# Optimization experiments

Measured on AMD Instinct MI355X. Metric: run time of the kernel, lower is better.

Reference implementation:

```python
import jax, jax.numpy as jnp
import numpy as np

D_MODEL = 512
N_HEADS = 8
HEAD_DIM = D_MODEL // N_HEADS
B, L, S = 4, 2048, 2048


def setup_inputs() -> dict:
    key = jax.random.key(0)
    ks = jax.random.split(key, 16)
    std = 1.0 / np.sqrt(D_MODEL)
    inp = {
        'queries': jax.random.normal(ks[0], (B, L, D_MODEL), jnp.float32),
        'keys': jax.random.normal(ks[1], (B, S, D_MODEL), jnp.float32),
        'values': jax.random.normal(ks[2], (B, S, D_MODEL), jnp.float32),
        'tau': jax.random.uniform(ks[3], (B,), jnp.float32, 0.5, 1.5),
        'delta': jax.random.normal(ks[4], (B,), jnp.float32) * 0.1,
        'Wq': jax.random.normal(ks[5], (D_MODEL, D_MODEL), jnp.float32) * std,
        'bq': jnp.zeros((D_MODEL,), jnp.float32),
        'Wk': jax.random.normal(ks[6], (D_MODEL, D_MODEL), jnp.float32) * std,
        'bk': jnp.zeros((D_MODEL,), jnp.float32),
        'Wv': jax.random.normal(ks[7], (D_MODEL, D_MODEL), jnp.float32) * std,
        'bv': jnp.zeros((D_MODEL,), jnp.float32),
        'Wo': jax.random.normal(ks[8], (D_MODEL, D_MODEL), jnp.float32) * std,
        'bo': jnp.zeros((D_MODEL,), jnp.float32),
    }
    return inp


def reference(queries, keys, values, tau, delta, Wq, bq, Wk, bk, Wv, bv, Wo, bo):
    Bq, Lq, _ = queries.shape
    Sk = keys.shape[1]
    H, E = N_HEADS, HEAD_DIM
    # projections -> [B, L, H, E]
    q = (queries @ Wq + bq).reshape(Bq, Lq, H, E)
    k = (keys @ Wk + bk).reshape(Bq, Sk, H, E)
    v = (values @ Wv + bv).reshape(Bq, Sk, H, E)
    scale = 1.0 / jnp.sqrt(jnp.float32(E))
    # scores: [B, H, L, S]
    scores = jnp.einsum('blhe,bshe->bhls', q, k)
    scores = scores * tau[:, None, None, None] + delta[:, None, None, None]
    A = jax.nn.softmax(scale * scores, axis=-1)  # dropout is identity in eval
    out = jnp.einsum('bhls,bshd->blhd', A, v).reshape(Bq, Lq, H * E)
    return out @ Wo + bo
```

## Files before the change

kernel.cpp:

```cpp
#include <hip/hip_runtime.h>
#include <stdint.h>

#define NB 4
#define LQ 2048
#define DM 512
#define NH 8
#define EH 64
#define MT (NB*LQ)
#define QBLK 128

typedef __attribute__((ext_vector_type(4)))  float f32x4;
typedef __attribute__((ext_vector_type(8)))  __bf16 bf16x8;
typedef __attribute__((ext_vector_type(8)))  unsigned short u16x8;
typedef __attribute__((ext_vector_type(4)))  float float4_t;
typedef __attribute__((ext_vector_type(2)))  unsigned int u32x2;

static __device__ __forceinline__ unsigned short f2bf(float f) {
  unsigned int u = __builtin_bit_cast(unsigned int, f);
  u += 0x7fffu + ((u >> 16) & 1u);
  return (unsigned short)(u >> 16);
}

static __device__ __forceinline__ float bf2f(unsigned short h) {
  unsigned int u = ((unsigned int)h) << 16;
  return __builtin_bit_cast(float, u);
}

static __device__ __forceinline__ void gload16(const void* g, void* l) {
  __builtin_amdgcn_global_load_lds(
      (__attribute__((address_space(1))) unsigned int*)(g),
      (__attribute__((address_space(3))) unsigned int*)(l), 16, 0, 0);
}

static __device__ __forceinline__ unsigned int cvt_pk_bf16(float lo, float hi) {
  unsigned int r;
  asm("v_cvt_pk_bf16_f32 %0, %1, %2" : "=v"(r) : "v"(lo), "v"(hi));
  return r;
}

extern "C" __global__ __launch_bounds__(256) void k_cast_x(
    const float* __restrict__ q, const float* __restrict__ k,
    const float* __restrict__ v, unsigned short* __restrict__ x) {
  int z = blockIdx.y;
  const float* src = (z == 0) ? q : ((z == 1) ? k : v);
  unsigned short* dst = x + (size_t)z * MT * DM;
  size_t i = ((size_t)blockIdx.x * 256 + threadIdx.x) * 8;
  float4_t a = *(const float4_t*)(src + i);
  float4_t b = *(const float4_t*)(src + i + 4);
  u16x8 r;
  r[0]=f2bf(a[0]); r[1]=f2bf(a[1]); r[2]=f2bf(a[2]); r[3]=f2bf(a[3]);
  r[4]=f2bf(b[0]); r[5]=f2bf(b[1]); r[6]=f2bf(b[2]); r[7]=f2bf(b[3]);
  *(u16x8*)(dst + i) = r;
}

extern "C" __global__ __launch_bounds__(256) void k_cast_wt(
    const float* __restrict__ wq, const float* __restrict__ wk,
    const float* __restrict__ wv, const float* __restrict__ wo,
    unsigned short* __restrict__ wt) {
  __shared__ float tile[64][65];
  int z = blockIdx.z;
  const float* w = (z==0)?wq : (z==1)?wk : (z==2)?wv : wo;
  unsigned short* dst = wt + (size_t)z * DM * DM;
  int kb = blockIdx.y * 64, nb = blockIdx.x * 64;
  int t = threadIdx.x;
  int r = t >> 2, c0 = (t & 3) * 16;
  #pragma unroll
  for (int i = 0; i < 16; i += 4) {
    float4_t v4 = *(const float4_t*)(w + (size_t)(kb + r) * DM + nb + c0 + i);
    tile[r][c0+i]   = v4[0]; tile[r][c0+i+1] = v4[1];
    tile[r][c0+i+2] = v4[2]; tile[r][c0+i+3] = v4[3];
  }
  __syncthreads();
  u16x8 o0, o1;
  #pragma unroll
  for (int i = 0; i < 8; ++i) o0[i] = f2bf(tile[c0+i][r]);
  #pragma unroll
  for (int i = 0; i < 8; ++i) o1[i] = f2bf(tile[c0+8+i][r]);
  *(u16x8*)(dst + (size_t)(nb + r) * DM + kb + c0)     = o0;
  *(u16x8*)(dst + (size_t)(nb + r) * DM + kb + c0 + 8) = o1;
}

extern "C" __global__ __launch_bounds__(256) void k_gemm_qkv(
    const unsigned short* __restrict__ X, const unsigned short* __restrict__ WT,
    const float* __restrict__ bq, const float* __restrict__ bk,
    const float* __restrict__ bv, const float* __restrict__ tau,
    unsigned short* __restrict__ out) {
  int z = blockIdx.z;
  const unsigned short* A  = X  + (size_t)z * MT * DM;
  const unsigned short* Bt = WT + (size_t)z * DM * DM;
  const float* bias = (z==0)?bq : (z==1)?bk : bv;
  unsigned short* dst = out + (size_t)z * MT * DM;

  __shared__ unsigned short As[2][128][32];
  __shared__ unsigned short Bs[2][128][32];

  int m0 = blockIdx.y * 128;
  int n0 = blockIdx.x * 128;
  float qsc = (z == 0) ? tau[m0 >> 11] * 0.18033688011112042f : 1.0f;
  int t = threadIdx.x;
  int lane = t & 63;
  int w = t >> 6;
  int wr = w >> 1, wc = w & 1;
  int g = lane >> 4, r15 = lane & 15;

  f32x4 acc[4][4];
  #pragma unroll
  for (int i=0;i<4;i++)
    #pragma unroll
    for (int j=0;j<4;j++)
      #pragma unroll
      for (int e=0;e<4;e++) acc[i][j][e] = 0.f;

  auto stage = [&](int bb, int kt) {
    int k0 = kt * 32;
    int sblk = (t & 3) ^ ((t >> 3) & 3);
    #pragma unroll
    for (int j=0;j<2;j++) {
      int o = t*16 + j*4096;
      int row = o >> 6;
      gload16(A  + (size_t)(m0+row)*DM + k0 + sblk*8, (char*)(&As[bb][0][0]) + o);
      gload16(Bt + (size_t)(n0+row)*DM + k0 + sblk*8, (char*)(&Bs[bb][0][0]) + o);
    }
  };

  stage(0, 0);
  __syncthreads();
  int buf = 0;
  for (int kt = 0; kt < DM/32; ++kt) {
    if (kt + 1 < DM/32) stage(buf ^ 1, kt + 1);
    bf16x8 af[4], bfr[4];
    #pragma unroll
    for (int mi=0;mi<4;mi++) {
      int row = wr*64 + mi*16 + r15;
      int blk = g ^ ((row >> 1) & 3);
      af[mi] = *(const bf16x8*)(&As[buf][row][blk*8]);
    }
    #pragma unroll
    for (int ni=0;ni<4;ni++) {
      int row = wc*64 + ni*16 + r15;
      int blk = g ^ ((row >> 1) & 3);
      bfr[ni] = *(const bf16x8*)(&Bs[buf][row][blk*8]);
    }
    #pragma unroll
    for (int mi=0;mi<4;mi++)
      #pragma unroll
      for (int ni=0;ni<4;ni++)
        acc[mi][ni] = __builtin_amdgcn_mfma_f32_16x16x32_bf16(af[mi], bfr[ni], acc[mi][ni], 0, 0, 0);
    __syncthreads();
    buf ^= 1;
  }
  #pragma unroll
  for (int ni=0;ni<4;ni++) {
    int n = n0 + wc*64 + ni*16 + r15;
    float bia = bias[n];
    int h = n >> 6, e = n & 63;
    #pragma unroll
    for (int mi=0;mi<4;mi++) {
      #pragma unroll
      for (int rg=0;rg<4;rg++) {
        int m = m0 + wr*64 + mi*16 + g*4 + rg;
        int b = m >> 11, s = m & 2047;
        dst[((size_t)((b*NH + h)*LQ + s))*EH + e] = f2bf((acc[mi][ni][rg] + bia) * qsc);
      }
    }
  }
}

extern "C" __global__ __launch_bounds__(256) void k_vt(
    const unsigned short* __restrict__ qkv, unsigned short* __restrict__ vtg) {
  __shared__ unsigned short tile[64][65];
  int bh = blockIdx.y;
  int s0 = blockIdx.x * 64;
  const unsigned short* Vh = qkv + (size_t)2*MT*DM + (size_t)bh*LQ*EH;
  unsigned short* Ot = vtg + (size_t)bh*EH*LQ;
  int t = threadIdx.x;
  int r = t >> 2, c0 = (t & 3) * 16;
  u16x8 a = *(const u16x8*)(Vh + (size_t)(s0 + r)*EH + c0);
  u16x8 b = *(const u16x8*)(Vh + (size_t)(s0 + r)*EH + c0 + 8);
  #pragma unroll
  for (int i=0;i<8;i++) { tile[r][c0+i] = a[i]; tile[r][c0+8+i] = b[i]; }
  __syncthreads();
  u16x8 o0, o1;
  #pragma unroll
  for (int i=0;i<8;i++) o0[i] = tile[c0+i][r];
  #pragma unroll
  for (int i=0;i<8;i++) o1[i] = tile[c0+8+i][r];
  *(u16x8*)(Ot + (size_t)r*LQ + s0 + c0)     = o0;
  *(u16x8*)(Ot + (size_t)r*LQ + s0 + c0 + 8) = o1;
}

template<int NSPLIT>
__global__ __launch_bounds__(256, 4) void k_flash(
    const unsigned short* __restrict__ qkv, const unsigned short* __restrict__ vtg,
    unsigned short* __restrict__ aout,
    unsigned short* __restrict__ opart, float* __restrict__ lpart) {
  constexpr int SKV = LQ / NSPLIT;
  constexpr int NIT = SKV / 32;
  constexpr int CPX = (512 * NSPLIT) / 8;
  int bid = blockIdx.x;
  int wgid = (bid & 7) * CPX + (bid >> 3);
  int part = wgid % NSPLIT;
  int rest = wgid / NSPLIT;
  int qblk = rest & 15;
  int bh = rest >> 4;
  int batch = bh >> 3, h = bh & 7;

  const unsigned short* Qh  = qkv + (size_t)bh * LQ * EH + (size_t)qblk * QBLK * EH;
  const unsigned short* Kh  = qkv + (size_t)MT * DM + (size_t)bh * LQ * EH + (size_t)part * SKV * EH;
  const unsigned short* VTh = vtg + (size_t)bh * EH * LQ + (size_t)part * SKV;

  __shared__ unsigned short Ks[2][32][64];
  __shared__ unsigned short Vt[2][64][32];
  __shared__ unsigned short Pall[4][32][40];

  int t = threadIdx.x;
  int lane = t & 63;
  int wv = t >> 6;
  int q4 = lane & 15;
  int g  = lane >> 4;

  unsigned short (*Pw)[40] = Pall[wv];

  auto stage = [&](int bb, int it) {
    int o = t * 16;
    int krow = t >> 3;
    int sblk = (t & 7) ^ ((krow ^ (krow >> 3)) & 7);
    gload16(Kh + (size_t)(it*32 + krow)*EH + sblk*8, (char*)(&Ks[bb][0][0]) + o);
    gload16(VTh + (size_t)(t >> 2)*LQ + it*32 + (t & 3)*8, (char*)(&Vt[bb][0][0]) + o);
  };

  bf16x8 qf[2][2];
  #pragma unroll
  for (int qt=0;qt<2;qt++)
    #pragma unroll
    for (int st=0;st<2;st++)
      qf[qt][st] = *(const bf16x8*)(Qh + (size_t)(wv*32 + qt*16 + q4)*EH + st*32 + g*8);

  stage(0, 0);

  union { unsigned short u[8]; bf16x8 v; } onesu;
  #pragma unroll
  for (int i=0;i<8;i++) onesu.u[i] = 0x3F80;
  const bf16x8 ones8 = onesu.v;

  const f32x4 Z4 = {0.f, 0.f, 0.f, 0.f};
  f32x4 oacc[4][2];
  #pragma unroll
  for (int a=0;a<4;a++)
    #pragma unroll
    for (int b2=0;b2<2;b2++)
      #pragma unroll
      for (int e=0;e<4;e++) oacc[a][b2][e] = 0.f;
  f32x4 ols[2];
  #pragma unroll
  for (int b2=0;b2<2;b2++)
    #pragma unroll
    for (int e=0;e<4;e++) ols[b2][e] = 0.f;

  __syncthreads();
  int buf = 0;
  for (int it = 0; it < NIT; ++it) {
    if (it + 1 < NIT) stage(buf ^ 1, it + 1);

    f32x4 sac[2][2];
    __builtin_amdgcn_s_setprio(1);
    #pragma unroll
    for (int kvt=0; kvt<2; ++kvt) {
      int row = kvt*16 + q4;
      int S = (row ^ (row >> 3)) & 7;
      bf16x8 kf0 = *(const bf16x8*)(&Ks[buf][row][(g ^ S)*8]);
      sac[kvt][0] = __builtin_amdgcn_mfma_f32_16x16x32_bf16(kf0, qf[0][0], Z4, 0,0,0);
      sac[kvt][1] = __builtin_amdgcn_mfma_f32_16x16x32_bf16(kf0, qf[1][0], Z4, 0,0,0);
    }
    #pragma unroll
    for (int kvt=0; kvt<2; ++kvt) {
      int row = kvt*16 + q4;
      int S = (row ^ (row >> 3)) & 7;
      bf16x8 kf1 = *(const bf16x8*)(&Ks[buf][row][((4 + g) ^ S)*8]);
      sac[kvt][0] = __builtin_amdgcn_mfma_f32_16x16x32_bf16(kf1, qf[0][1], sac[kvt][0], 0,0,0);
      sac[kvt][1] = __builtin_amdgcn_mfma_f32_16x16x32_bf16(kf1, qf[1][1], sac[kvt][1], 0,0,0);
    }
    __builtin_amdgcn_s_setprio(0);

    #pragma unroll
    for (int qt=0; qt<2; ++qt) {
      int qrow = qt*16 + q4;
      #pragma unroll
      for (int kvt=0; kvt<2; ++kvt) {
        float p0 = __builtin_amdgcn_exp2f(sac[kvt][qt][0]);
        float p1 = __builtin_amdgcn_exp2f(sac[kvt][qt][1]);
        float p2 = __builtin_amdgcn_exp2f(sac[kvt][qt][2]);
        float p3 = __builtin_amdgcn_exp2f(sac[kvt][qt][3]);
        u32x2 wpk;
        wpk[0] = cvt_pk_bf16(p0, p1);
        wpk[1] = cvt_pk_bf16(p2, p3);
        *(u32x2*)(&Pw[qrow][kvt*16 + g*4]) = wpk;
      }
    }
    asm volatile("s_waitcnt lgkmcnt(0)" ::: "memory");
    __builtin_amdgcn_sched_barrier(0);

    bf16x8 pf[2];
    #pragma unroll
    for (int qt=0; qt<2; ++qt)
      pf[qt] = *(const bf16x8*)(&Pw[qt*16 + q4][g*8]);
    __builtin_amdgcn_s_setprio(1);
    #pragma unroll
    for (int et=0; et<4; ++et) {
      bf16x8 vf = *(const bf16x8*)(&Vt[buf][et*16 + q4][g*8]);
      oacc[et][0] = __builtin_amdgcn_mfma_f32_16x16x32_bf16(vf, pf[0], oacc[et][0], 0,0,0);
      oacc[et][1] = __builtin_amdgcn_mfma_f32_16x16x32_bf16(vf, pf[1], oacc[et][1], 0,0,0);
    }
    ols[0] = __builtin_amdgcn_mfma_f32_16x16x32_bf16(ones8, pf[0], ols[0], 0,0,0);
    ols[1] = __builtin_amdgcn_mfma_f32_16x16x32_bf16(ones8, pf[1], ols[1], 0,0,0);
    __builtin_amdgcn_s_setprio(0);

    __syncthreads();
    buf ^= 1;
  }

  #pragma unroll
  for (int qt=0; qt<2; ++qt) {
    float s = ols[qt][0];
    int q = qblk*QBLK + wv*32 + qt*16 + q4;
    if constexpr (NSPLIT == 1) {
      float inv = 1.f / s;
      unsigned short* rowp = aout + (size_t)(batch*LQ + q)*DM + h*EH;
      #pragma unroll
      for (int et=0; et<4; ++et) {
        #pragma unroll
        for (int rg=0; rg<4; rg+=2) {
          int e = et*16 + g*4 + rg;
          *(unsigned int*)(rowp + e) = cvt_pk_bf16(oacc[et][qt][rg] * inv, oacc[et][qt][rg+1] * inv);
        }
      }
    } else {
      size_t r = (size_t)bh * LQ + q;
      unsigned short* od = opart + ((size_t)r*NSPLIT + part) * 64;
      #pragma unroll
      for (int et=0; et<4; ++et) {
        u32x2 wpk;
        wpk[0] = cvt_pk_bf16(oacc[et][qt][0], oacc[et][qt][1]);
        wpk[1] = cvt_pk_bf16(oacc[et][qt][2], oacc[et][qt][3]);
        *(u32x2*)(od + et*16 + g*4) = wpk;
      }
      if (g == 0) lpart[r*NSPLIT + part] = s;
    }
  }
}

extern "C" __global__ __launch_bounds__(256) void k_red(
    const unsigned short* __restrict__ op, const float* __restrict__ lp,
    unsigned short* __restrict__ aout) {
  int t = threadIdx.x;
  int r = blockIdx.x * 16 + (t >> 4);
  int e0 = (t & 15) * 4;
  float acc0 = 0.f, acc1 = 0.f, acc2 = 0.f, acc3 = 0.f, ls = 0.f;
  #pragma unroll
  for (int qq = 0; qq < 4; ++qq) {
    u32x2 wv = *(const u32x2*)(op + ((size_t)r*4 + qq)*64 + e0);
    acc0 += bf2f((unsigned short)(wv[0] & 0xFFFF));
    acc1 += bf2f((unsigned short)(wv[0] >> 16));
    acc2 += bf2f((unsigned short)(wv[1] & 0xFFFF));
    acc3 += bf2f((unsigned short)(wv[1] >> 16));
    ls += lp[(size_t)r*4 + qq];
  }
  float inv = 1.f / ls;
  int bh = r >> 11, q = r & 2047, batch = bh >> 3, h = bh & 7;
  unsigned short* dst = aout + (size_t)(batch*LQ + q)*DM + h*EH + e0;
  u32x2 w;
  w[0] = cvt_pk_bf16(acc0 * inv, acc1 * inv);
  w[1] = cvt_pk_bf16(acc2 * inv, acc3 * inv);
  *(u32x2*)dst = w;
}

extern "C" __global__ __launch_bounds__(256) void k_gemm_out(
    const unsigned short* __restrict__ A, const unsigned short* __restrict__ WT,
    const float* __restrict__ bo, float* __restrict__ out) {
  const unsigned short* Bt = WT + (size_t)3 * DM * DM;

  __shared__ unsigned short As[2][128][32];
  __shared__ unsigned short Bs[2][128][32];

  int m0 = blockIdx.y * 128;
  int n0 = blockIdx.x * 128;
  int t = threadIdx.x;
  int lane = t & 63;
  int w = t >> 6;
  int wr = w >> 1, wc = w & 1;
  int g = lane >> 4, r15 = lane & 15;

  f32x4 acc[4][4];
  #pragma unroll
  for (int i=0;i<4;i++)
    #pragma unroll
    for (int j=0;j<4;j++)
      #pragma unroll
      for (int e=0;e<4;e++) acc[i][j][e] = 0.f;

  auto stage = [&](int bb, int kt) {
    int k0 = kt * 32;
    int sblk = (t & 3) ^ ((t >> 3) & 3);
    #pragma unroll
    for (int j=0;j<2;j++) {
      int o = t*16 + j*4096;
      int row = o >> 6;
      gload16(A  + (size_t)(m0+row)*DM + k0 + sblk*8, (char*)(&As[bb][0][0]) + o);
      gload16(Bt + (size_t)(n0+row)*DM + k0 + sblk*8, (char*)(&Bs[bb][0][0]) + o);
    }
  };

  stage(0, 0);
  __syncthreads();
  int buf = 0;
  for (int kt = 0; kt < DM/32; ++kt) {
    if (kt + 1 < DM/32) stage(buf ^ 1, kt + 1);
    bf16x8 af[4], bfr[4];
    #pragma unroll
    for (int mi=0;mi<4;mi++) {
      int row = wr*64 + mi*16 + r15;
      int blk = g ^ ((row >> 1) & 3);
      af[mi] = *(const bf16x8*)(&As[buf][row][blk*8]);
    }
    #pragma unroll
    for (int ni=0;ni<4;ni++) {
      int row = wc*64 + ni*16 + r15;
      int blk = g ^ ((row >> 1) & 3);
      bfr[ni] = *(const bf16x8*)(&Bs[buf][row][blk*8]);
    }
    #pragma unroll
    for (int mi=0;mi<4;mi++)
      #pragma unroll
      for (int ni=0;ni<4;ni++)
        acc[mi][ni] = __builtin_amdgcn_mfma_f32_16x16x32_bf16(af[mi], bfr[ni], acc[mi][ni], 0, 0, 0);
    __syncthreads();
    buf ^= 1;
  }
  #pragma unroll
  for (int ni=0;ni<4;ni++) {
    int n = n0 + wc*64 + ni*16 + r15;
    float bia = bo[n];
    #pragma unroll
    for (int mi=0;mi<4;mi++) {
      #pragma unroll
      for (int rg=0;rg<4;rg++) {
        int m = m0 + wr*64 + mi*16 + g*4 + rg;
        out[(size_t)m*DM + n] = acc[mi][ni][rg] + bia;
      }
    }
  }
}

extern "C" void kernel_launch(void* const* d_in, const int* in_sizes, int n_in,
                              void* d_out, int out_size, void* d_ws, size_t ws_size,
                              hipStream_t stream) {
  const float* queries = (const float*)d_in[0];
  const float* keys    = (const float*)d_in[1];
  const float* values  = (const float*)d_in[2];
  const float* tau     = (const float*)d_in[3];
  const float* Wq = (const float*)d_in[5];
  const float* bq = (const float*)d_in[6];
  const float* Wk = (const float*)d_in[7];
  const float* bk = (const float*)d_in[8];
  const float* Wv = (const float*)d_in[9];
  const float* bv = (const float*)d_in[10];
  const float* Wo = (const float*)d_in[11];
  const float* bo = (const float*)d_in[12];
  float* out = (float*)d_out;

  char* ws = (char*)d_ws;
  unsigned short* WT   = (unsigned short*)(ws);
  unsigned short* X    = (unsigned short*)(ws + (2u  << 20));
  unsigned short* VTg  = (unsigned short*)(ws + (2u  << 20));
  unsigned short* AOut = (unsigned short*)(ws + (10u << 20));
  unsigned short* QKV  = (unsigned short*)(ws + (26u << 20));
  unsigned short* Opart= (unsigned short*)(ws + (50u << 20));
  float*          Lpart= (float*)(ws + (84u << 20));

  k_cast_x  <<<dim3(2048, 3), dim3(256), 0, stream>>>(queries, keys, values, X);
  k_cast_wt <<<dim3(8, 8, 4), dim3(256), 0, stream>>>(Wq, Wk, Wv, Wo, WT);
  k_gemm_qkv<<<dim3(4, 64, 3), dim3(256), 0, stream>>>(X, WT, bq, bk, bv, tau, QKV);
  k_vt      <<<dim3(32, 32), dim3(256), 0, stream>>>(QKV, VTg);

  if (ws_size >= ((size_t)85u << 20)) {
    k_flash<4><<<dim3(2048), dim3(256), 0, stream>>>(QKV, VTg, AOut, Opart, Lpart);
    k_red    <<<dim3(4096), dim3(256), 0, stream>>>(Opart, Lpart, AOut);
  } else {
    k_flash<1><<<dim3(512), dim3(256), 0, stream>>>(QKV, VTg, AOut, Opart, Lpart);
  }
  k_gemm_out<<<dim3(4, 64), dim3(256), 0, stream>>>(AOut, WT, bo, out);
}
```

Before: 116.8 us.

## Feed P from registers via 16x16x16 MFMA, drop LDS P round-trip

Softmax probabilities are kept in registers and fed directly as B operands to 16x16x16 bf16 MFMAs. This removes the per-iteration LDS write/read of P and the lgkmcnt wait. To make that work, the V transpose kernel now writes V^T in a permuted, swizzled column order that matches the register layout of P. The row-sum now comes from per-lane accumulation plus two cross-lane shuffles at the end instead of ones-vector MFMAs. The trade is twice as many MFMA instructions, each half the K depth, and a more intricate layout contract between the two kernels.

```diff
diff --git a/kernel.cpp b/kernel.cpp
--- a/kernel.cpp
+++ b/kernel.cpp
@@ -12,6 +12,7 @@
 typedef __attribute__((ext_vector_type(4)))  float f32x4;
 typedef __attribute__((ext_vector_type(8)))  __bf16 bf16x8;
 typedef __attribute__((ext_vector_type(8)))  unsigned short u16x8;
+typedef __attribute__((ext_vector_type(4)))  short s16x4;
 typedef __attribute__((ext_vector_type(4)))  float float4_t;
 typedef __attribute__((ext_vector_type(2)))  unsigned int u32x2;
 
@@ -36,6 +37,22 @@
   unsigned int r;
   asm("v_cvt_pk_bf16_f32 %0, %1, %2" : "=v"(r) : "v"(lo), "v"(hi));
   return r;
+}
+
+static __device__ __forceinline__ f32x4 mfma16(s16x4 a, s16x4 b, f32x4 c) {
+#if defined(__HIP_DEVICE_COMPILE__)
+#if __has_builtin(__builtin_amdgcn_mfma_f32_16x16x16bf16_1k)
+  return __builtin_amdgcn_mfma_f32_16x16x16bf16_1k(a, b, c, 0, 0, 0);
+#else
+  f32x4 d;
+  asm volatile("v_mfma_f32_16x16x16_bf16 %0, %1, %2, %3"
+               : "=v"(d) : "v"(a), "v"(b), "0"(c));
+  return d;
+#endif
+#else
+  (void)a; (void)b;
+  return c;
+#endif
 }
 
 extern "C" __global__ __launch_bounds__(256) void k_cast_x(
@@ -180,13 +197,19 @@
   #pragma unroll
   for (int i=0;i<8;i++) { tile[r][c0+i] = a[i]; tile[r][c0+8+i] = b[i]; }
   __syncthreads();
-  u16x8 o0, o1;
-  #pragma unroll
-  for (int i=0;i<8;i++) o0[i] = tile[c0+i][r];
-  #pragma unroll
-  for (int i=0;i<8;i++) o1[i] = tile[c0+8+i][r];
-  *(u16x8*)(Ot + (size_t)r*LQ + s0 + c0)     = o0;
-  *(u16x8*)(Ot + (size_t)r*LQ + s0 + c0 + 8) = o1;
+  int gg = t & 3;
+  int er = t >> 2;
+  int s2 = (er ^ (er >> 3)) & 3;
+  #pragma unroll
+  for (int blk = 0; blk < 2; ++blk) {
+    u16x8 o;
+    #pragma unroll
+    for (int j = 0; j < 8; ++j) {
+      int sp = blk*32 + (j >> 2)*16 + gg*4 + (j & 3);
+      o[j] = tile[sp][er];
+    }
+    *(u16x8*)(Ot + (size_t)er*LQ + s0 + blk*32 + 8*(gg ^ s2)) = o;
+  }
 }
 
 template<int NSPLIT>
@@ -211,15 +234,12 @@
 
   __shared__ unsigned short Ks[2][32][64];
   __shared__ unsigned short Vt[2][64][32];
-  __shared__ unsigned short Pall[4][32][40];
 
   int t = threadIdx.x;
   int lane = t & 63;
   int wv = t >> 6;
   int q4 = lane & 15;
   int g  = lane >> 4;
-
-  unsigned short (*Pw)[40] = Pall[wv];
 
   auto stage = [&](int bb, int it) {
     int o = t * 16;
@@ -238,11 +258,6 @@
 
   stage(0, 0);
 
-  union { unsigned short u[8]; bf16x8 v; } onesu;
-  #pragma unroll
-  for (int i=0;i<8;i++) onesu.u[i] = 0x3F80;
-  const bf16x8 ones8 = onesu.v;
-
   const f32x4 Z4 = {0.f, 0.f, 0.f, 0.f};
   f32x4 oacc[4][2];
   #pragma unroll
@@ -251,11 +266,7 @@
     for (int b2=0;b2<2;b2++)
       #pragma unroll
       for (int e=0;e<4;e++) oacc[a][b2][e] = 0.f;
-  f32x4 ols[2];
-  #pragma unroll
-  for (int b2=0;b2<2;b2++)
-    #pragma unroll
-    for (int e=0;e<4;e++) ols[b2][e] = 0.f;
+  float lsp[2] = {0.f, 0.f};
 
   __syncthreads();
   int buf = 0;
@@ -282,37 +293,35 @@
     }
     __builtin_amdgcn_s_setprio(0);
 
+    s16x4 pk[2][2];
     #pragma unroll
     for (int qt=0; qt<2; ++qt) {
-      int qrow = qt*16 + q4;
       #pragma unroll
       for (int kvt=0; kvt<2; ++kvt) {
         float p0 = __builtin_amdgcn_exp2f(sac[kvt][qt][0]);
         float p1 = __builtin_amdgcn_exp2f(sac[kvt][qt][1]);
         float p2 = __builtin_amdgcn_exp2f(sac[kvt][qt][2]);
         float p3 = __builtin_amdgcn_exp2f(sac[kvt][qt][3]);
-        u32x2 wpk;
-        wpk[0] = cvt_pk_bf16(p0, p1);
-        wpk[1] = cvt_pk_bf16(p2, p3);
-        *(u32x2*)(&Pw[qrow][kvt*16 + g*4]) = wpk;
+        lsp[qt] += (p0 + p1) + (p2 + p3);
+        union { u32x2 u; s16x4 h; } pu;
+        pu.u[0] = cvt_pk_bf16(p0, p1);
+        pu.u[1] = cvt_pk_bf16(p2, p3);
+        pk[qt][kvt] = pu.h;
       }
     }
-    asm volatile("s_waitcnt lgkmcnt(0)" ::: "memory");
-    __builtin_amdgcn_sched_barrier(0);
-
-    bf16x8 pf[2];
-    #pragma unroll
-    for (int qt=0; qt<2; ++qt)
-      pf[qt] = *(const bf16x8*)(&Pw[qt*16 + q4][g*8]);
+
     __builtin_amdgcn_s_setprio(1);
     #pragma unroll
     for (int et=0; et<4; ++et) {
-      bf16x8 vf = *(const bf16x8*)(&Vt[buf][et*16 + q4][g*8]);
-      oacc[et][0] = __builtin_amdgcn_mfma_f32_16x16x32_bf16(vf, pf[0], oacc[et][0], 0,0,0);
-      oacc[et][1] = __builtin_amdgcn_mfma_f32_16x16x32_bf16(vf, pf[1], oacc[et][1], 0,0,0);
-    }
-    ols[0] = __builtin_amdgcn_mfma_f32_16x16x32_bf16(ones8, pf[0], ols[0], 0,0,0);
-    ols[1] = __builtin_amdgcn_mfma_f32_16x16x32_bf16(ones8, pf[1], ols[1], 0,0,0);
+      int row = et*16 + q4;
+      int s2 = (row ^ (row >> 3)) & 3;
+      union { u16x8 w; s16x4 h[2]; } vu;
+      vu.w = *(const u16x8*)(&Vt[buf][row][(g ^ s2)*8]);
+      oacc[et][0] = mfma16(vu.h[0], pk[0][0], oacc[et][0]);
+      oacc[et][0] = mfma16(vu.h[1], pk[0][1], oacc[et][0]);
+      oacc[et][1] = mfma16(vu.h[0], pk[1][0], oacc[et][1]);
+      oacc[et][1] = mfma16(vu.h[1], pk[1][1], oacc[et][1]);
+    }
     __builtin_amdgcn_s_setprio(0);
 
     __syncthreads();
@@ -321,7 +330,9 @@
 
   #pragma unroll
   for (int qt=0; qt<2; ++qt) {
-    float s = ols[qt][0];
+    float s = lsp[qt];
+    s += __shfl_xor(s, 16, 64);
+    s += __shfl_xor(s, 32, 64);
     int q = qblk*QBLK + wv*32 + qt*16 + q4;
     if constexpr (NSPLIT == 1) {
       float inv = 1.f / s;
```

New measurement: 117.4 us. Within noise of the previous version (+0.5%).
